# Kernel optimization log

Measured on AMD Instinct MI355X. Metric: run time of the kernel, lower is better.

The kernel has to match this reference:

```python
import jax, jax.numpy as jnp
import numpy as np

FEAT_DIM = 1024
NUM_HEADS = 16
HEAD_DIM = FEAT_DIM // NUM_HEADS
B, T = 8, 1024


def setup_inputs() -> dict:
    key = jax.random.key(0)
    k_x, k_wqkv, k_bqkv, k_wp, k_bp = jax.random.split(key, 5)
    s = 1.0 / np.sqrt(FEAT_DIM)
    return {
        "x": jax.random.normal(k_x, (B, T, FEAT_DIM), dtype=jnp.float32),
        "padding_mask": jnp.zeros((B, T), dtype=bool),  # True = padded position
        "W_qkv": jax.random.normal(k_wqkv, (3 * FEAT_DIM, FEAT_DIM), dtype=jnp.float32) * s,
        "b_qkv": jax.random.normal(k_bqkv, (3 * FEAT_DIM,), dtype=jnp.float32) * 0.01,
        "W_proj": jax.random.normal(k_wp, (FEAT_DIM, FEAT_DIM), dtype=jnp.float32) * s,
        "b_proj": jax.random.normal(k_bp, (FEAT_DIM,), dtype=jnp.float32) * 0.01,
        "scale_factor": jnp.asarray(1.0 / np.sqrt(HEAD_DIM), dtype=jnp.float32),
    }


def reference(x, padding_mask, W_qkv, b_qkv, W_proj, b_proj, scale_factor):
    Bb, Tt, D = x.shape
    H, hd = NUM_HEADS, HEAD_DIM
    # fused QKV projection: [B,T,3D] -> [3,B,H,T,hd]
    qkv = (x @ W_qkv.T + b_qkv).reshape(Bb, Tt, 3, H, hd).transpose(2, 0, 3, 1, 4)
    q, k, v = qkv[0], qkv[1], qkv[2]
    # scores [B,H,T,T]
    attn = jnp.einsum("bhqd,bhkd->bhqk", q, k) * scale_factor
    causal = jnp.triu(jnp.ones((Tt, Tt), dtype=bool), k=1)  # [T,T]
    mask = causal[None, None] | padding_mask[:, None, None, :]  # [B,H,T,T] via broadcast
    attn = jnp.where(mask, -jnp.inf, attn)
    attn = jax.nn.softmax(attn, axis=-1)
    # dropout is identity in eval mode
    out = jnp.einsum("bhqk,bhkd->bqhd", attn, v).reshape(Bb, Tt, D)
    return out @ W_proj.T + b_proj
```

## Files before the change

### kernel.cpp

```cpp
#include <hip/hip_runtime.h>
#include <cstdint>
#include <cstddef>

typedef unsigned short u16;
typedef __attribute__((ext_vector_type(2))) unsigned short u16x2;
typedef __attribute__((ext_vector_type(4))) unsigned short u16x4;
typedef __attribute__((ext_vector_type(8))) unsigned short u16x8;
typedef __attribute__((ext_vector_type(8))) short s16x8;
typedef __attribute__((ext_vector_type(4))) float f32x4;

__device__ __forceinline__ u16 f2bf(float f) {
  uint32_t u = __float_as_uint(f);
  u += 0x7fffu + ((u >> 16) & 1u);
  return (u16)(u >> 16);
}

__device__ __forceinline__ f32x4 mfma16(s16x8 a, s16x8 b, f32x4 c) {
  return __builtin_amdgcn_mfma_f32_16x16x32_bf16(a, b, c, 0, 0, 0);
}

#define GLDS16(gp, lp) __builtin_amdgcn_global_load_lds(                     \
    (const __attribute__((address_space(1))) void*)(gp),                      \
    (__attribute__((address_space(3))) void*)(lp), 16, 0, 0)

__global__ void cvt_f32_bf16(const float* __restrict__ in, u16* __restrict__ out, int n4) {
  int stride = gridDim.x * blockDim.x;
  for (int i = blockIdx.x * blockDim.x + threadIdx.x; i < n4; i += stride) {
    f32x4 v = ((const f32x4*)in)[i];
    u16x4 o;
    o[0] = f2bf(v[0]); o[1] = f2bf(v[1]); o[2] = f2bf(v[2]); o[3] = f2bf(v[3]);
    ((u16x4*)out)[i] = o;
  }
}

template <int OUT_BF16>
__global__ __launch_bounds__(256, 2)
void gemm_bt(const u16* __restrict__ A, const u16* __restrict__ B,
             const float* __restrict__ bias, u16* __restrict__ Cb,
             float* __restrict__ Cf, int M, int N, int K, int tilesN) {
  __shared__ u16 lA[128 * 32];
  __shared__ u16 lB[128 * 32];

  int bid = blockIdx.x;
  int cpx = gridDim.x >> 3;
  bid = (bid & 7) * cpx + (bid >> 3);

  const int tm = bid / tilesN, tn = bid % tilesN;
  const int row0 = tm * 128, col0 = tn * 128;
  const int tid = threadIdx.x;
  const int lane = tid & 63, wave = tid >> 6;

  const u16* Ag = A + (size_t)(row0 + (tid >> 2)) * K + (tid & 3) * 8;
  const u16* Bg = B + (size_t)(col0 + (tid >> 2)) * K + (tid & 3) * 8;
  const int ldsoff = tid * 8;

  const int wm = (wave >> 1) * 64, wn = (wave & 1) * 64;
  const int fr = lane & 15, fk = (lane >> 4) * 8;

  f32x4 acc[4][4] = {};

  for (int k0 = 0; k0 < K; k0 += 32) {
    __syncthreads();
    GLDS16(Ag + k0, &lA[ldsoff]);
    GLDS16(Ag + (size_t)64 * K + k0, &lA[2048 + ldsoff]);
    GLDS16(Bg + k0, &lB[ldsoff]);
    GLDS16(Bg + (size_t)64 * K + k0, &lB[2048 + ldsoff]);
    __syncthreads();

    s16x8 af[4], bfr[4];
#pragma unroll
    for (int i = 0; i < 4; ++i) af[i] = *(const s16x8*)&lA[(wm + i * 16 + fr) * 32 + fk];
#pragma unroll
    for (int i = 0; i < 4; ++i) bfr[i] = *(const s16x8*)&lB[(wn + i * 16 + fr) * 32 + fk];
#pragma unroll
    for (int i = 0; i < 4; ++i)
#pragma unroll
      for (int j = 0; j < 4; ++j) acc[i][j] = mfma16(af[i], bfr[j], acc[i][j]);
  }

#pragma unroll
  for (int i = 0; i < 4; ++i) {
#pragma unroll
    for (int r = 0; r < 4; ++r) {
      const int row = row0 + wm + i * 16 + (lane >> 4) * 4 + r;
#pragma unroll
      for (int j = 0; j < 4; ++j) {
        const int col = col0 + wn + j * 16 + fr;
        const float v = acc[i][j][r] + bias[col];
        if (OUT_BF16)
          Cb[(size_t)row * N + col] = f2bf(v);
        else
          Cf[(size_t)row * N + col] = v;
      }
    }
  }
}

__global__ __launch_bounds__(256)
void vtrans(const u16* __restrict__ qkv, u16* __restrict__ vt) {
  __shared__ u16 lT[64][68];
  const int bid = blockIdx.x;
  const int bh = bid >> 4;
  const int tt = bid & 15;
  const int b = bh >> 4, h = bh & 15;
  const int tid = threadIdx.x;
  const int row = tid >> 2;
  const int cc = (tid & 3) * 16;

  const u16* src = qkv + (size_t)(b * 1024 + tt * 64 + row) * 3072 + 2048 + h * 64 + cc;
  *(u16x8*)&lT[row][cc] = *(const u16x8*)src;
  *(u16x8*)&lT[row][cc + 8] = *(const u16x8*)(src + 8);
  __syncthreads();

  u16 tmp[16];
#pragma unroll
  for (int i = 0; i < 16; ++i) tmp[i] = lT[cc + i][row];
  u16* dst = vt + (size_t)(bh * 64 + row) * 1024 + tt * 64 + cc;
  *(u16x8*)dst = *(u16x8*)&tmp[0];
  *(u16x8*)(dst + 8) = *(u16x8*)&tmp[8];
}

__global__ __launch_bounds__(256)
void attn2(const u16* __restrict__ qkv, const u16* __restrict__ vt,
           const unsigned char* __restrict__ pmask,
           const float* __restrict__ scale_ptr, u16* __restrict__ outp) {
  __shared__ u16 lP[4][32 * 72];
  const int tid = threadIdx.x;
  const int lane = tid & 63, wave = tid >> 6;
  const int fr = lane & 15, grp = lane >> 4;
  const int w = blockIdx.x * 4 + wave;
  const int qc = 31 - (w >> 7);
  const int bh = w & 127;
  const int b = bh >> 4, h = bh & 15;
  const int qb = qc * 32;
  const float scale = scale_ptr[0];

  const u16* Kbase = qkv + (size_t)b * 1024 * 3072 + 1024 + h * 64;
  const u16* Vbase = vt + (size_t)bh * 64 * 1024;
  u16* lp = &lP[wave][0];

  s16x8 qf[2][2];
#pragma unroll
  for (int g = 0; g < 2; ++g)
#pragma unroll
    for (int c = 0; c < 2; ++c)
      qf[g][c] = *(const s16x8*)(qkv + (size_t)(b * 1024 + qb + g * 16 + fr) * 3072 +
                                 h * 64 + c * 32 + grp * 8);

  f32x4 oacc[2][4] = {};
  float m_run[2] = {-1e30f, -1e30f};
  float l_run[2] = {0.0f, 0.0f};

  const int ntiles = (qc >> 1) + 1;
  for (int t = 0; t < ntiles; ++t) {
    const int kvb = t * 64;

    f32x4 st[4][2] = {};
#pragma unroll
    for (int f = 0; f < 4; ++f) {
      const u16* kp = Kbase + (size_t)(kvb + f * 16 + fr) * 3072 + grp * 8;
      s16x8 ka0 = *(const s16x8*)kp;
      s16x8 ka1 = *(const s16x8*)(kp + 32);
      st[f][0] = mfma16(ka0, qf[0][0], st[f][0]);
      st[f][0] = mfma16(ka1, qf[0][1], st[f][0]);
      st[f][1] = mfma16(ka0, qf[1][0], st[f][1]);
      st[f][1] = mfma16(ka1, qf[1][1], st[f][1]);
    }

    uint32_t pm[4];
#pragma unroll
    for (int f = 0; f < 4; ++f)
      pm[f] = *(const uint32_t*)(pmask + b * 1024 + kvb + f * 16 + grp * 4);

    float ar[2][4];
#pragma unroll
    for (int g = 0; g < 2; ++g) {
      const int q = qb + g * 16 + fr;
      float tmax = -1e30f;
#pragma unroll
      for (int f = 0; f < 4; ++f)
#pragma unroll
        for (int r = 0; r < 4; ++r) {
          const int kv = kvb + f * 16 + grp * 4 + r;
          float v = st[f][g][r] * scale;
          const bool pad = ((pm[f] >> (8 * r)) & 0xff) != 0;
          v = (kv > q || pad) ? -1e30f : v;
          st[f][g][r] = v;
          tmax = fmaxf(tmax, v);
        }
      tmax = fmaxf(tmax, __shfl_xor(tmax, 16));
      tmax = fmaxf(tmax, __shfl_xor(tmax, 32));
      const float m_new = fmaxf(m_run[g], tmax);
      const float alpha = __expf(m_run[g] - m_new);

      float rsum = 0.0f;
#pragma unroll
      for (int f = 0; f < 4; ++f)
#pragma unroll
        for (int rp = 0; rp < 2; ++rp) {
          const float p0 = __expf(st[f][g][rp * 2 + 0] - m_new);
          const float p1 = __expf(st[f][g][rp * 2 + 1] - m_new);
          rsum += p0 + p1;
          u16x2 pk;
          pk[0] = f2bf(p0);
          pk[1] = f2bf(p1);
          *(u16x2*)&lp[(g * 16 + fr) * 72 + f * 16 + grp * 4 + rp * 2] = pk;
        }
      rsum += __shfl_xor(rsum, 16);
      rsum += __shfl_xor(rsum, 32);
      l_run[g] = l_run[g] * alpha + rsum;
      m_run[g] = m_new;
#pragma unroll
      for (int r = 0; r < 4; ++r) ar[g][r] = __shfl(alpha, grp * 4 + r);
    }

    s16x8 pa[2][2];
#pragma unroll
    for (int g = 0; g < 2; ++g)
#pragma unroll
      for (int kc = 0; kc < 2; ++kc)
        pa[g][kc] = *(const s16x8*)&lp[(g * 16 + fr) * 72 + kc * 32 + grp * 8];
#pragma unroll
    for (int nf = 0; nf < 4; ++nf) {
      const u16* vp = Vbase + (size_t)(nf * 16 + fr) * 1024 + kvb + grp * 8;
      s16x8 vb0 = *(const s16x8*)vp;
      s16x8 vb1 = *(const s16x8*)(vp + 32);
#pragma unroll
      for (int g = 0; g < 2; ++g) {
        f32x4 o = oacc[g][nf];
        o[0] *= ar[g][0];
        o[1] *= ar[g][1];
        o[2] *= ar[g][2];
        o[3] *= ar[g][3];
        o = mfma16(pa[g][0], vb0, o);
        o = mfma16(pa[g][1], vb1, o);
        oacc[g][nf] = o;
      }
    }
  }

#pragma unroll
  for (int g = 0; g < 2; ++g) {
    float linv[4];
#pragma unroll
    for (int r = 0; r < 4; ++r) linv[r] = 1.0f / __shfl(l_run[g], grp * 4 + r);
#pragma unroll
    for (int nf = 0; nf < 4; ++nf)
#pragma unroll
      for (int r = 0; r < 4; ++r) {
        const int tq = qb + g * 16 + grp * 4 + r;
        outp[(size_t)(b * 1024 + tq) * 1024 + h * 64 + nf * 16 + fr] =
            f2bf(oacc[g][nf][r] * linv[r]);
      }
  }
}

extern "C" void kernel_launch(void* const* d_in, const int* in_sizes, int n_in,
                              void* d_out, int out_size, void* d_ws, size_t ws_size,
                              hipStream_t stream) {
  const float* x = (const float*)d_in[0];
  const unsigned char* pmask = (const unsigned char*)d_in[1];
  const float* Wqkv = (const float*)d_in[2];
  const float* bqkv = (const float*)d_in[3];
  const float* Wproj = (const float*)d_in[4];
  const float* bproj = (const float*)d_in[5];
  const float* scale = (const float*)d_in[6];
  float* out = (float*)d_out;

  char* ws = (char*)d_ws;
  u16* xb     = (u16*)(ws + 0);
  u16* vtb    = (u16*)(ws + 0);
  u16* wqkvb  = (u16*)(ws + 16777216);
  u16* wprojb = (u16*)(ws + 23068672);
  u16* qkv    = (u16*)(ws + 25165824);
  u16* attno  = (u16*)(ws + 75497472);
  if (ws_size < (size_t)92274688) return;

  cvt_f32_bf16<<<2048, 256, 0, stream>>>(x, xb, 8 * 1024 * 1024 / 4);
  cvt_f32_bf16<<<1024, 256, 0, stream>>>(Wqkv, wqkvb, 3 * 1024 * 1024 / 4);
  cvt_f32_bf16<<<512, 256, 0, stream>>>(Wproj, wprojb, 1024 * 1024 / 4);

  gemm_bt<1><<<64 * 24, 256, 0, stream>>>(xb, wqkvb, bqkv, qkv, nullptr,
                                          8192, 3072, 1024, 24);
  vtrans<<<2048, 256, 0, stream>>>(qkv, vtb);
  attn2<<<1024, 256, 0, stream>>>(qkv, vtb, pmask, scale, attno);
  gemm_bt<0><<<64 * 8, 256, 0, stream>>>(attno, wprojb, bproj, nullptr, out,
                                         8192, 1024, 1024, 8);
}
```

Before: 276.6 us.

## Restructure attention loop with causal tile split, lazy rescale, and fused conversions

Merges the three fp32-to-bf16 conversion launches into one kernel. The attention kernel is split into full 64-wide unmasked tiles, an optional 32-wide unmasked tile and a final 32-wide causal diagonal tile. This skips the masked half-tile work and per-element causal compares on off-diagonal tiles. The padding mask is precomputed into an additive bias in LDS and applied with an FMA. Output rescaling is deferred unless the running max grows by more than a threshold, and bf16 packing uses a perm instruction with round-half-up instead of round-to-even. These trade a little numerical exactness for fewer ALU and MFMA operations.

After: 266.7 us. 3.6% less time.

```diff
diff --git a/kernel.cpp b/kernel.cpp
--- a/kernel.cpp
+++ b/kernel.cpp
@@ -23,13 +23,27 @@
     (const __attribute__((address_space(1))) void*)(gp),                      \
     (__attribute__((address_space(3))) void*)(lp), 16, 0, 0)
 
-__global__ void cvt_f32_bf16(const float* __restrict__ in, u16* __restrict__ out, int n4) {
-  int stride = gridDim.x * blockDim.x;
-  for (int i = blockIdx.x * blockDim.x + threadIdx.x; i < n4; i += stride) {
-    f32x4 v = ((const f32x4*)in)[i];
+__global__ void cvt_all(const float* __restrict__ x, const float* __restrict__ wq,
+                        const float* __restrict__ wp, u16* __restrict__ xb,
+                        u16* __restrict__ wqb, u16* __restrict__ wpb) {
+  const int n4x = 2097152, n4q = 786432, n4p = 262144;
+  const int total = n4x + n4q + n4p;
+  const int stride = gridDim.x * blockDim.x;
+  for (int i = blockIdx.x * blockDim.x + threadIdx.x; i < total; i += stride) {
+    const float* src;
+    u16* dst;
+    int j = i;
+    if (j < n4x) {
+      src = x; dst = xb;
+    } else if (j < n4x + n4q) {
+      j -= n4x; src = wq; dst = wqb;
+    } else {
+      j -= n4x + n4q; src = wp; dst = wpb;
+    }
+    f32x4 v = ((const f32x4*)src)[j];
     u16x4 o;
     o[0] = f2bf(v[0]); o[1] = f2bf(v[1]); o[2] = f2bf(v[2]); o[3] = f2bf(v[3]);
-    ((u16x4*)out)[i] = o;
+    ((u16x4*)dst)[j] = o;
   }
 }
 
@@ -120,11 +134,121 @@
   *(u16x8*)(dst + 8) = *(u16x8*)&tmp[8];
 }
 
+template <int NF, bool CAUSAL>
+__device__ __forceinline__ void attn_step(
+    const u16* __restrict__ Kbase, const u16* __restrict__ Vbase,
+    const float* __restrict__ pb, u16* __restrict__ lp, int kvb, int qb,
+    int fr, int grp, const s16x8 qf[2][2], f32x4 oacc[2][4], float m2[2],
+    float l2[2], float cs) {
+  f32x4 st[NF][2];
+#pragma unroll
+  for (int f = 0; f < NF; ++f) {
+    const u16* kp = Kbase + (size_t)(kvb + f * 16 + fr) * 3072 + grp * 8;
+    s16x8 ka0 = *(const s16x8*)kp;
+    s16x8 ka1 = *(const s16x8*)(kp + 32);
+    f32x4 a0 = {0.f, 0.f, 0.f, 0.f}, a1 = {0.f, 0.f, 0.f, 0.f};
+    a0 = mfma16(ka0, qf[0][0], a0);
+    a0 = mfma16(ka1, qf[0][1], a0);
+    a1 = mfma16(ka0, qf[1][0], a1);
+    a1 = mfma16(ka1, qf[1][1], a1);
+    st[f][0] = a0;
+    st[f][1] = a1;
+  }
+
+  f32x4 pbv[NF];
+#pragma unroll
+  for (int f = 0; f < NF; ++f)
+    pbv[f] = *(const f32x4*)&pb[kvb + f * 16 + grp * 4];
+
+  float tm[2];
+#pragma unroll
+  for (int g = 0; g < 2; ++g) {
+    const int q = qb + g * 16 + fr;
+    float t = -3.0e38f;
+#pragma unroll
+    for (int f = 0; f < NF; ++f)
+#pragma unroll
+      for (int r = 0; r < 4; ++r) {
+        float v = __builtin_fmaf(st[f][g][r], cs, pbv[f][r]);
+        if (CAUSAL) {
+          const int kv = kvb + f * 16 + grp * 4 + r;
+          v = (kv > q) ? -3.0e38f : v;
+        }
+        st[f][g][r] = v;
+        t = fmaxf(t, v);
+      }
+    t = fmaxf(t, __shfl_xor(t, 16));
+    t = fmaxf(t, __shfl_xor(t, 32));
+    tm[g] = t;
+  }
+
+  const bool defer = __all((tm[0] <= m2[0] + 8.0f) && (tm[1] <= m2[1] + 8.0f)) != 0;
+  if (!defer) {
+#pragma unroll
+    for (int g = 0; g < 2; ++g) {
+      const float mn = fmaxf(m2[g], tm[g]);
+      const float al = __expf(m2[g] - mn);
+      m2[g] = mn;
+      l2[g] *= al;
+      float ar[4];
+#pragma unroll
+      for (int r = 0; r < 4; ++r) ar[r] = __shfl(al, grp * 4 + r);
+#pragma unroll
+      for (int nf = 0; nf < 4; ++nf) {
+        oacc[g][nf][0] *= ar[0];
+        oacc[g][nf][1] *= ar[1];
+        oacc[g][nf][2] *= ar[2];
+        oacc[g][nf][3] *= ar[3];
+      }
+    }
+  }
+
+#pragma unroll
+  for (int g = 0; g < 2; ++g) {
+    float rsum = 0.f;
+#pragma unroll
+    for (int f = 0; f < NF; ++f)
+#pragma unroll
+      for (int rp = 0; rp < 2; ++rp) {
+        const float p0 = __expf(st[f][g][2 * rp] - m2[g]);
+        const float p1 = __expf(st[f][g][2 * rp + 1] - m2[g]);
+        rsum += p0 + p1;
+        const uint32_t pk = __builtin_amdgcn_perm(
+            __float_as_uint(p1) + 0x8000u, __float_as_uint(p0) + 0x8000u,
+            0x07060302u);
+        *(uint32_t*)&lp[(g * 16 + fr) * 72 + f * 16 + grp * 4 + 2 * rp] = pk;
+      }
+    rsum += __shfl_xor(rsum, 16);
+    rsum += __shfl_xor(rsum, 32);
+    l2[g] += rsum;
+  }
+
+  s16x8 pa[2][NF / 2];
+#pragma unroll
+  for (int g = 0; g < 2; ++g)
+#pragma unroll
+    for (int kc = 0; kc < NF / 2; ++kc)
+      pa[g][kc] = *(const s16x8*)&lp[(g * 16 + fr) * 72 + kc * 32 + grp * 8];
+#pragma unroll
+  for (int nf = 0; nf < 4; ++nf) {
+    const u16* vp = Vbase + (size_t)(nf * 16 + fr) * 1024 + kvb + grp * 8;
+    s16x8 vb0 = *(const s16x8*)vp;
+#pragma unroll
+    for (int g = 0; g < 2; ++g) {
+      f32x4 o = oacc[g][nf];
+      o = mfma16(pa[g][0], vb0, o);
+      if (NF == 4) o = mfma16(pa[g][1], *(const s16x8*)(vp + 32), o);
+      oacc[g][nf] = o;
+    }
+  }
+}
+
 __global__ __launch_bounds__(256)
-void attn2(const u16* __restrict__ qkv, const u16* __restrict__ vt,
+void attn3(const u16* __restrict__ qkv, const u16* __restrict__ vt,
            const unsigned char* __restrict__ pmask,
            const float* __restrict__ scale_ptr, u16* __restrict__ outp) {
   __shared__ u16 lP[4][32 * 72];
+  __shared__ float lPb[1024];
   const int tid = threadIdx.x;
   const int lane = tid & 63, wave = tid >> 6;
   const int fr = lane & 15, grp = lane >> 4;
@@ -133,7 +257,11 @@
   const int bh = w & 127;
   const int b = bh >> 4, h = bh & 15;
   const int qb = qc * 32;
-  const float scale = scale_ptr[0];
+  const float cs = scale_ptr[0];
+
+  for (int i = tid; i < 1024; i += 256)
+    lPb[i] = pmask[b * 1024 + i] ? -3.0e38f : 0.0f;
+  __syncthreads();
 
   const u16* Kbase = qkv + (size_t)b * 1024 * 3072 + 1024 + h * 64;
   const u16* Vbase = vt + (size_t)bh * 64 * 1024;
@@ -148,102 +276,21 @@
                                  h * 64 + c * 32 + grp * 8);
 
   f32x4 oacc[2][4] = {};
-  float m_run[2] = {-1e30f, -1e30f};
-  float l_run[2] = {0.0f, 0.0f};
-
-  const int ntiles = (qc >> 1) + 1;
-  for (int t = 0; t < ntiles; ++t) {
-    const int kvb = t * 64;
-
-    f32x4 st[4][2] = {};
-#pragma unroll
-    for (int f = 0; f < 4; ++f) {
-      const u16* kp = Kbase + (size_t)(kvb + f * 16 + fr) * 3072 + grp * 8;
-      s16x8 ka0 = *(const s16x8*)kp;
-      s16x8 ka1 = *(const s16x8*)(kp + 32);
-      st[f][0] = mfma16(ka0, qf[0][0], st[f][0]);
-      st[f][0] = mfma16(ka1, qf[0][1], st[f][0]);
-      st[f][1] = mfma16(ka0, qf[1][0], st[f][1]);
-      st[f][1] = mfma16(ka1, qf[1][1], st[f][1]);
-    }
-
-    uint32_t pm[4];
-#pragma unroll
-    for (int f = 0; f < 4; ++f)
-      pm[f] = *(const uint32_t*)(pmask + b * 1024 + kvb + f * 16 + grp * 4);
-
-    float ar[2][4];
-#pragma unroll
-    for (int g = 0; g < 2; ++g) {
-      const int q = qb + g * 16 + fr;
-      float tmax = -1e30f;
-#pragma unroll
-      for (int f = 0; f < 4; ++f)
-#pragma unroll
-        for (int r = 0; r < 4; ++r) {
-          const int kv = kvb + f * 16 + grp * 4 + r;
-          float v = st[f][g][r] * scale;
-          const bool pad = ((pm[f] >> (8 * r)) & 0xff) != 0;
-          v = (kv > q || pad) ? -1e30f : v;
-          st[f][g][r] = v;
-          tmax = fmaxf(tmax, v);
-        }
-      tmax = fmaxf(tmax, __shfl_xor(tmax, 16));
-      tmax = fmaxf(tmax, __shfl_xor(tmax, 32));
-      const float m_new = fmaxf(m_run[g], tmax);
-      const float alpha = __expf(m_run[g] - m_new);
-
-      float rsum = 0.0f;
-#pragma unroll
-      for (int f = 0; f < 4; ++f)
-#pragma unroll
-        for (int rp = 0; rp < 2; ++rp) {
-          const float p0 = __expf(st[f][g][rp * 2 + 0] - m_new);
-          const float p1 = __expf(st[f][g][rp * 2 + 1] - m_new);
-          rsum += p0 + p1;
-          u16x2 pk;
-          pk[0] = f2bf(p0);
-          pk[1] = f2bf(p1);
-          *(u16x2*)&lp[(g * 16 + fr) * 72 + f * 16 + grp * 4 + rp * 2] = pk;
-        }
-      rsum += __shfl_xor(rsum, 16);
-      rsum += __shfl_xor(rsum, 32);
-      l_run[g] = l_run[g] * alpha + rsum;
-      m_run[g] = m_new;
-#pragma unroll
-      for (int r = 0; r < 4; ++r) ar[g][r] = __shfl(alpha, grp * 4 + r);
-    }
-
-    s16x8 pa[2][2];
-#pragma unroll
-    for (int g = 0; g < 2; ++g)
-#pragma unroll
-      for (int kc = 0; kc < 2; ++kc)
-        pa[g][kc] = *(const s16x8*)&lp[(g * 16 + fr) * 72 + kc * 32 + grp * 8];
-#pragma unroll
-    for (int nf = 0; nf < 4; ++nf) {
-      const u16* vp = Vbase + (size_t)(nf * 16 + fr) * 1024 + kvb + grp * 8;
-      s16x8 vb0 = *(const s16x8*)vp;
-      s16x8 vb1 = *(const s16x8*)(vp + 32);
-#pragma unroll
-      for (int g = 0; g < 2; ++g) {
-        f32x4 o = oacc[g][nf];
-        o[0] *= ar[g][0];
-        o[1] *= ar[g][1];
-        o[2] *= ar[g][2];
-        o[3] *= ar[g][3];
-        o = mfma16(pa[g][0], vb0, o);
-        o = mfma16(pa[g][1], vb1, o);
-        oacc[g][nf] = o;
-      }
-    }
-  }
+  float m2[2] = {-1e30f, -1e30f};
+  float l2[2] = {0.0f, 0.0f};
+
+  const int FT = qc >> 1;
+  for (int t = 0; t < FT; ++t)
+    attn_step<4, false>(Kbase, Vbase, lPb, lp, t * 64, qb, fr, grp, qf, oacc, m2, l2, cs);
+  if (qc & 1)
+    attn_step<2, false>(Kbase, Vbase, lPb, lp, qb - 32, qb, fr, grp, qf, oacc, m2, l2, cs);
+  attn_step<2, true>(Kbase, Vbase, lPb, lp, qb, qb, fr, grp, qf, oacc, m2, l2, cs);
 
 #pragma unroll
   for (int g = 0; g < 2; ++g) {
     float linv[4];
 #pragma unroll
-    for (int r = 0; r < 4; ++r) linv[r] = 1.0f / __shfl(l_run[g], grp * 4 + r);
+    for (int r = 0; r < 4; ++r) linv[r] = 1.0f / __shfl(l2[g], grp * 4 + r);
 #pragma unroll
     for (int nf = 0; nf < 4; ++nf)
 #pragma unroll
@@ -276,14 +323,12 @@
   u16* attno  = (u16*)(ws + 75497472);
   if (ws_size < (size_t)92274688) return;
 
-  cvt_f32_bf16<<<2048, 256, 0, stream>>>(x, xb, 8 * 1024 * 1024 / 4);
-  cvt_f32_bf16<<<1024, 256, 0, stream>>>(Wqkv, wqkvb, 3 * 1024 * 1024 / 4);
-  cvt_f32_bf16<<<512, 256, 0, stream>>>(Wproj, wprojb, 1024 * 1024 / 4);
+  cvt_all<<<2048, 256, 0, stream>>>(x, Wqkv, Wproj, xb, wqkvb, wprojb);
 
   gemm_bt<1><<<64 * 24, 256, 0, stream>>>(xb, wqkvb, bqkv, qkv, nullptr,
                                           8192, 3072, 1024, 24);
   vtrans<<<2048, 256, 0, stream>>>(qkv, vtb);
-  attn2<<<1024, 256, 0, stream>>>(qkv, vtb, pmask, scale, attno);
+  attn3<<<1024, 256, 0, stream>>>(qkv, vtb, pmask, scale, attno);
   gemm_bt<0><<<64 * 8, 256, 0, stream>>>(attno, wprojb, bproj, nullptr, out,
                                          8192, 1024, 1024, 8);
 }
```
